# Performance work log

Hardware: AMD Instinct MI355X
Metric: run time of the kernel (lower is better)

Reference implementation:

```python
import jax, jax.numpy as jnp
import numpy as np

B, T, C = 2, 2048, 1024
H = 4 * C           # MLP hidden (4*n_embd)
E_DYN = 7           # num_experts - static_experts
TOP_K = 2           # num_experts_per_tok
MOE_LOSS_COEF = 0.01


def setup_inputs() -> dict:
    key = jax.random.key(0)
    ks = jax.random.split(key, 6)
    s = 0.02
    x = jax.random.normal(ks[0], (B, T, C), dtype=jnp.float32)
    gate_w = jax.random.normal(ks[1], (C, E_DYN), dtype=jnp.float32) * s
    w1 = jax.random.normal(ks[2], (E_DYN, C, H), dtype=jnp.float32) * s   # dynamic experts c_fc
    w2 = jax.random.normal(ks[3], (E_DYN, H, C), dtype=jnp.float32) * s   # dynamic experts c_proj
    w1s = jax.random.normal(ks[4], (C, H), dtype=jnp.float32) * s         # static expert c_fc
    w2s = jax.random.normal(ks[5], (H, C), dtype=jnp.float32) * s         # static expert c_proj
    return {"x": x, "gate_w": gate_w, "w1": w1, "w2": w2, "w1s": w1s, "w2s": w2s}


def reference(x, gate_w, w1, w2, w1s, w2s):
    b, t, c = x.shape
    xf = x.reshape(-1, c)                                   # [N, C]
    n = xf.shape[0]

    # static expert (always applied)
    y_static = jax.nn.gelu(xf @ w1s, approximate=False) @ w2s  # [N, C]

    # gating: top-k + softmax over selected scores
    scores = xf @ gate_w                                    # [N, E]
    topk_scores, topk_idx = jax.lax.top_k(scores, TOP_K)    # [N, K]
    topk_w = jax.nn.softmax(topk_scores, axis=-1)           # [N, K]

    # dense dispatch weights [N, E] (top_k indices are distinct -> set is safe)
    probs = jnp.zeros((n, E_DYN), dtype=x.dtype)
    probs = probs.at[jnp.arange(n)[:, None], topk_idx].set(topk_w)

    # all-expert MLP then weighted combine (same math as masked per-expert dispatch)
    h = jax.nn.gelu(jnp.einsum('nc,ech->enh', xf, w1), approximate=False)  # [E, N, H]
    y_all = jnp.einsum('enh,ehc->enc', h, w2)               # [E, N, C]
    y_dyn = jnp.einsum('ne,enc->nc', probs, y_all)          # [N, C]

    y = (y_dyn + y_static).reshape(b, t, c)

    # variance_penalty auxiliary loss
    expert_usage = probs.mean(axis=0)                       # [E]
    variance = jnp.mean((expert_usage - expert_usage.mean()) ** 2)
    aux = MOE_LOSS_COEF * variance
    return y, aux
```

## Files before the change

### kernel.cpp

```cpp
#include <hip/hip_runtime.h>
#include <hip/hip_bf16.h>
#include <math.h>

#define N_TOK 4096
#define C_DIM 1024
#define H_DIM 4096
#define NEXP 7
#define NGRP 8
#define HCAP 13184

typedef __attribute__((ext_vector_type(8))) short short8;
typedef __attribute__((ext_vector_type(4))) float floatx4;

static const size_t OFF_COUNTS = 0;
static const size_t OFF_CURSOR = 64;
static const size_t OFF_BASE   = 128;
static const size_t OFF_PCOUNT = 192;
static const size_t OFF_CNT8   = 256;
static const size_t OFF_USAGE  = 320;
static const size_t OFF_TOPKI  = 4096;
static const size_t OFF_TOPKW  = OFF_TOPKI + 8192ull * 4;
static const size_t OFF_ETOK   = OFF_TOPKW + 8192ull * 4;
static const size_t OFF_EWT    = OFF_ETOK + (size_t)HCAP * 4;
static const size_t OFF_XB     = 262144;
static const size_t OFF_W1T    = OFF_XB + (size_t)N_TOK * C_DIM * 2;
static const size_t OFF_W2T    = OFF_W1T + (size_t)NGRP * H_DIM * C_DIM * 2;
static const size_t OFF_H      = OFF_W2T + (size_t)NGRP * C_DIM * H_DIM * 2;

static __device__ __forceinline__ unsigned short f2bf(float f) {
    __hip_bfloat16 b = __float2bfloat16(f);
    return *reinterpret_cast<unsigned short*>(&b);
}

static __device__ __forceinline__ void gll16(const void* g, void* l) {
    __builtin_amdgcn_global_load_lds((const __attribute__((address_space(1))) void*)g,
                                     (__attribute__((address_space(3))) void*)l, 16, 0, 0);
}

__global__ void init_small_kernel(int* counts, int* cursor, float* usage) {
    int i = threadIdx.x;
    if (i < 8) { counts[i] = 0; cursor[i] = 0; usage[i] = 0.f; }
}

__global__ void zero_out_kernel(float* y, int n) {
    int i = blockIdx.x * blockDim.x + threadIdx.x;
    int stride = gridDim.x * blockDim.x;
    for (; i < n; i += stride) y[i] = 0.f;
}

__global__ void convert_x_kernel(const float* __restrict__ x, unsigned short* __restrict__ xb) {
    int i = blockIdx.x * 256 + threadIdx.x;
    float4 v = ((const float4*)x)[i];
    ushort4 o;
    o.x = f2bf(v.x); o.y = f2bf(v.y); o.z = f2bf(v.z); o.w = f2bf(v.w);
    ((ushort4*)xb)[i] = o;
}

__global__ __launch_bounds__(256) void transpose_cvt_kernel(
    const float* __restrict__ dyn, const float* __restrict__ stat,
    __hip_bfloat16* __restrict__ dst, int R, int S)
{
    int e = blockIdx.z;
    const float* src = (e < NEXP) ? (dyn + (size_t)e * R * S) : stat;
    __hip_bfloat16* d = dst + (size_t)e * R * S;
    int s0 = blockIdx.x * 32, r0 = blockIdx.y * 64;
    int tx = threadIdx.x & 31, ty = threadIdx.x >> 5;
    __shared__ float t[64][33];
#pragma unroll
    for (int i = 0; i < 8; i++) {
        int r = ty + i * 8;
        t[r][tx] = src[(size_t)(r0 + r) * S + s0 + tx];
    }
    __syncthreads();
    int tx2 = threadIdx.x & 63, ty2 = threadIdx.x >> 6;
#pragma unroll
    for (int i = 0; i < 8; i++) {
        int s = ty2 + i * 4;
        d[(size_t)(s0 + s) * R + r0 + tx2] = __float2bfloat16(t[tx2][s]);
    }
}

__global__ __launch_bounds__(256) void gate_kernel(
    const float* __restrict__ x, const float* __restrict__ gw,
    int* __restrict__ topki, float* __restrict__ topkw,
    int* counts, float* usage)
{
    int wid = threadIdx.x >> 6, lane = threadIdx.x & 63;
    int t = blockIdx.x * 4 + wid;
    float s[NEXP];
#pragma unroll
    for (int e = 0; e < NEXP; e++) s[e] = 0.f;
    for (int c = lane; c < C_DIM; c += 64) {
        float xv = x[(size_t)t * C_DIM + c];
#pragma unroll
        for (int e = 0; e < NEXP; e++) s[e] += xv * gw[c * NEXP + e];
    }
#pragma unroll
    for (int e = 0; e < NEXP; e++)
        for (int off = 32; off > 0; off >>= 1) s[e] += __shfl_xor(s[e], off);
    if (lane == 0) {
        int e0 = 0;
        for (int e = 1; e < NEXP; e++) if (s[e] > s[e0]) e0 = e;
        int e1 = -1;
        for (int e = 0; e < NEXP; e++) {
            if (e == e0) continue;
            if (e1 < 0 || s[e] > s[e1]) e1 = e;
        }
        float w0 = 1.f / (1.f + expf(s[e1] - s[e0]));
        float w1 = 1.f - w0;
        topki[t * 2] = e0; topki[t * 2 + 1] = e1;
        topkw[t * 2] = w0; topkw[t * 2 + 1] = w1;
        atomicAdd(&counts[e0], 1); atomicAdd(&counts[e1], 1);
        atomicAdd(&usage[e0], w0); atomicAdd(&usage[e1], w1);
    }
}

__global__ __launch_bounds__(256) void prefix_kernel(
    const int* counts, const float* usage,
    int* base, int* pcount, int* cnt8,
    int* etok, float* ewt, float* y, int aux_index)
{
    __shared__ int sb[NGRP], sc[NGRP], sp[NGRP];
    if (threadIdx.x == 0) {
        int run = 0;
        for (int g = 0; g < NEXP; g++) {
            int c = counts[g];
            int p = (c + 127) & ~127;
            base[g] = run; pcount[g] = p; cnt8[g] = c;
            sb[g] = run; sc[g] = c; sp[g] = p;
            run += p;
        }
        base[NEXP] = run; pcount[NEXP] = N_TOK; cnt8[NEXP] = N_TOK;
        sb[NEXP] = run; sc[NEXP] = N_TOK; sp[NEXP] = N_TOK;
        float u[NEXP]; float mean = 0.f;
        for (int e = 0; e < NEXP; e++) { u[e] = usage[e] / (float)N_TOK; mean += u[e]; }
        mean /= (float)NEXP;
        float var = 0.f;
        for (int e = 0; e < NEXP; e++) { float d = u[e] - mean; var += d * d; }
        var /= (float)NEXP;
        y[aux_index] = 0.01f * var;
    }
    __syncthreads();
    for (int i = threadIdx.x; i < N_TOK; i += 256) {
        etok[sb[NEXP] + i] = i; ewt[sb[NEXP] + i] = 1.0f;
    }
    for (int g = 0; g < NEXP; g++) {
        for (int i = sc[g] + (int)threadIdx.x; i < sp[g]; i += 256) {
            etok[sb[g] + i] = 0; ewt[sb[g] + i] = 0.f;
        }
    }
}

__global__ void scatter_kernel(const int* __restrict__ topki, const float* __restrict__ topkw,
                               const int* __restrict__ base, int* cursor,
                               int* __restrict__ etok, float* __restrict__ ewt)
{
    int i = blockIdx.x * 256 + threadIdx.x;
    int t = i >> 1;
    int e = topki[i];
    float w = topkw[i];
    int pos = atomicAdd(&cursor[e], 1);
    int idx = base[e] + pos;
    etok[idx] = t; ewt[idx] = w;
}

__global__ __launch_bounds__(256) void gemm1_kernel(
    const __hip_bfloat16* __restrict__ xb,
    const __hip_bfloat16* __restrict__ w1t,
    __hip_bfloat16* __restrict__ h,
    const int* __restrict__ etok,
    const int* __restrict__ base,
    const int* __restrict__ pcount)
{
    int g = blockIdx.z, mt = blockIdx.y, ct = blockIdx.x;
    if (mt * 128 >= pcount[g]) return;
    int eb = base[g];

    __shared__ __align__(16) char AlsB[2 * 8192];
    __shared__ __align__(16) char BlsB[2 * 8192];

    int tid = threadIdx.x;
    int lane = tid & 63, wid = tid >> 6;
    int quad = lane >> 4, l16 = lane & 15;
    int wm = wid >> 1, wn = wid & 1;
    int rsub = lane >> 2, chunk = lane & 3;

    const char* gA[2]; const char* gB[2];
    char* lA[2]; char* lB[2];
#pragma unroll
    for (int j = 0; j < 2; j++) {
        int rowA = wid * 32 + j * 16 + rsub;
        int tok = etok[eb + mt * 128 + rowA];
        gA[j] = (const char*)(xb + (size_t)tok * C_DIM) + chunk * 16;
        lA[j] = AlsB + (wid * 32 + j * 16) * 64;
        int rowB = wid * 32 + j * 16 + rsub;
        gB[j] = (const char*)(w1t + ((size_t)g * H_DIM + ct * 128 + rowB) * C_DIM) + chunk * 16;
        lB[j] = BlsB + (wid * 32 + j * 16) * 64;
    }

    floatx4 acc[4][4] = {};
    for (int k0 = 0; k0 < C_DIM; k0 += 64) {
        size_t koff = (size_t)k0 * 2;
#pragma unroll
        for (int s = 0; s < 2; s++) {
            size_t so = koff + (size_t)s * 64;
            gll16(gA[0] + so, lA[0] + s * 8192);
            gll16(gA[1] + so, lA[1] + s * 8192);
            gll16(gB[0] + so, lB[0] + s * 8192);
            gll16(gB[1] + so, lB[1] + s * 8192);
        }
        __syncthreads();
#pragma unroll
        for (int s = 0; s < 2; s++) {
            short8 a[4], b[4];
#pragma unroll
            for (int i = 0; i < 4; i++) {
                a[i] = *(const short8*)(AlsB + s * 8192 + (((wm * 64 + i * 16 + l16) * 32 + quad * 8) * 2));
                b[i] = *(const short8*)(BlsB + s * 8192 + (((wn * 64 + i * 16 + l16) * 32 + quad * 8) * 2));
            }
#pragma unroll
            for (int i = 0; i < 4; i++)
#pragma unroll
                for (int j = 0; j < 4; j++)
                    acc[i][j] = __builtin_amdgcn_mfma_f32_16x16x32_bf16(a[i], b[j], acc[i][j], 0, 0, 0);
        }
        __syncthreads();
    }

#pragma unroll
    for (int i = 0; i < 4; i++) {
        int rbase = mt * 128 + wm * 64 + i * 16 + quad * 4;
#pragma unroll
        for (int reg = 0; reg < 4; reg++) {
            size_t hrow = (size_t)(eb + rbase + reg) * H_DIM;
#pragma unroll
            for (int j = 0; j < 4; j++) {
                int cc = ct * 128 + wn * 64 + j * 16 + l16;
                float v = acc[i][j][reg];
                float ge = 0.5f * v * (1.0f + erff(v * 0.70710678118654752f));
                h[hrow + cc] = __float2bfloat16(ge);
            }
        }
    }
}

__global__ __launch_bounds__(256) void gemm2_kernel(
    const __hip_bfloat16* __restrict__ h,
    const __hip_bfloat16* __restrict__ w2t,
    float* __restrict__ y,
    const int* __restrict__ etok,
    const float* __restrict__ ewt,
    const int* __restrict__ base,
    const int* __restrict__ pcount,
    const int* __restrict__ cnt8)
{
    int g = blockIdx.z, ct = blockIdx.x, mt = blockIdx.y;
    if (mt * 128 >= pcount[g]) return;
    int eb = base[g];
    int cnt = cnt8[g];

    __shared__ __align__(16) char AlsB[2 * 8192];
    __shared__ __align__(16) char BlsB[2 * 8192];

    int tid = threadIdx.x;
    int lane = tid & 63, wid = tid >> 6;
    int quad = lane >> 4, l16 = lane & 15;
    int wm = wid >> 1, wn = wid & 1;
    int rsub = lane >> 2, chunk = lane & 3;

    const char* gA[2]; const char* gB[2];
    char* lA[2]; char* lB[2];
#pragma unroll
    for (int j = 0; j < 2; j++) {
        int rowA = wid * 32 + j * 16 + rsub;
        gA[j] = (const char*)(h + (size_t)(eb + mt * 128 + rowA) * H_DIM) + chunk * 16;
        lA[j] = AlsB + (wid * 32 + j * 16) * 64;
        int rowB = wid * 32 + j * 16 + rsub;
        gB[j] = (const char*)(w2t + ((size_t)g * C_DIM + ct * 128 + rowB) * H_DIM) + chunk * 16;
        lB[j] = BlsB + (wid * 32 + j * 16) * 64;
    }

    floatx4 acc[4][4] = {};
    for (int k0 = 0; k0 < H_DIM; k0 += 64) {
        size_t koff = (size_t)k0 * 2;
#pragma unroll
        for (int s = 0; s < 2; s++) {
            size_t so = koff + (size_t)s * 64;
            gll16(gA[0] + so, lA[0] + s * 8192);
            gll16(gA[1] + so, lA[1] + s * 8192);
            gll16(gB[0] + so, lB[0] + s * 8192);
            gll16(gB[1] + so, lB[1] + s * 8192);
        }
        __syncthreads();
#pragma unroll
        for (int s = 0; s < 2; s++) {
            short8 a[4], b[4];
#pragma unroll
            for (int i = 0; i < 4; i++) {
                a[i] = *(const short8*)(AlsB + s * 8192 + (((wm * 64 + i * 16 + l16) * 32 + quad * 8) * 2));
                b[i] = *(const short8*)(BlsB + s * 8192 + (((wn * 64 + i * 16 + l16) * 32 + quad * 8) * 2));
            }
#pragma unroll
            for (int i = 0; i < 4; i++)
#pragma unroll
                for (int j = 0; j < 4; j++)
                    acc[i][j] = __builtin_amdgcn_mfma_f32_16x16x32_bf16(a[i], b[j], acc[i][j], 0, 0, 0);
        }
        __syncthreads();
    }

#pragma unroll
    for (int i = 0; i < 4; i++) {
        int rl0 = mt * 128 + wm * 64 + i * 16 + quad * 4;
#pragma unroll
        for (int reg = 0; reg < 4; reg++) {
            int rl = rl0 + reg;
            if (rl < cnt) {
                int entry = eb + rl;
                float w = ewt[entry];
                int tok = etok[entry];
                size_t yrow = (size_t)tok * C_DIM;
#pragma unroll
                for (int j = 0; j < 4; j++) {
                    int cc = ct * 128 + wn * 64 + j * 16 + l16;
                    atomicAdd(&y[yrow + cc], acc[i][j][reg] * w);
                }
            }
        }
    }
}

extern "C" void kernel_launch(void* const* d_in, const int* in_sizes, int n_in,
                              void* d_out, int out_size, void* d_ws, size_t ws_size,
                              hipStream_t stream) {
    const float* x      = (const float*)d_in[0];
    const float* gate_w = (const float*)d_in[1];
    const float* w1     = (const float*)d_in[2];
    const float* w2     = (const float*)d_in[3];
    const float* w1s    = (const float*)d_in[4];
    const float* w2s    = (const float*)d_in[5];
    float* y = (float*)d_out;
    char* ws = (char*)d_ws;

    int*   counts = (int*)(ws + OFF_COUNTS);
    int*   cursor = (int*)(ws + OFF_CURSOR);
    int*   base   = (int*)(ws + OFF_BASE);
    int*   pcount = (int*)(ws + OFF_PCOUNT);
    int*   cnt8   = (int*)(ws + OFF_CNT8);
    float* usage  = (float*)(ws + OFF_USAGE);
    int*   topki  = (int*)(ws + OFF_TOPKI);
    float* topkw  = (float*)(ws + OFF_TOPKW);
    int*   etok   = (int*)(ws + OFF_ETOK);
    float* ewt    = (float*)(ws + OFF_EWT);
    unsigned short* xb_u = (unsigned short*)(ws + OFF_XB);
    __hip_bfloat16* xb  = (__hip_bfloat16*)(ws + OFF_XB);
    __hip_bfloat16* w1t = (__hip_bfloat16*)(ws + OFF_W1T);
    __hip_bfloat16* w2t = (__hip_bfloat16*)(ws + OFF_W2T);
    __hip_bfloat16* hbuf = (__hip_bfloat16*)(ws + OFF_H);

    init_small_kernel<<<1, 64, 0, stream>>>(counts, cursor, usage);
    zero_out_kernel<<<2048, 256, 0, stream>>>(y, out_size);

    convert_x_kernel<<<(N_TOK * C_DIM / 4) / 256, 256, 0, stream>>>(x, xb_u);
    transpose_cvt_kernel<<<dim3(H_DIM / 32, C_DIM / 64, NGRP), 256, 0, stream>>>(w1, w1s, w1t, C_DIM, H_DIM);
    transpose_cvt_kernel<<<dim3(C_DIM / 32, H_DIM / 64, NGRP), 256, 0, stream>>>(w2, w2s, w2t, H_DIM, C_DIM);

    gate_kernel<<<N_TOK / 4, 256, 0, stream>>>(x, gate_w, topki, topkw, counts, usage);
    prefix_kernel<<<1, 256, 0, stream>>>(counts, usage, base, pcount, cnt8, etok, ewt, y, N_TOK * C_DIM);
    scatter_kernel<<<(N_TOK * 2) / 256, 256, 0, stream>>>(topki, topkw, base, cursor, etok, ewt);

    gemm1_kernel<<<dim3(H_DIM / 128, 64, NGRP), 256, 0, stream>>>(xb, w1t, hbuf, etok, base, pcount);
    gemm2_kernel<<<dim3(C_DIM / 128, 64, NGRP), 256, 0, stream>>>(hbuf, w2t, y, etok, ewt, base, pcount, cnt8);
}
```

Baseline: 838.1 us.

## Replace atomic scatter-add in gemm2 with per-row partial writes and combine kernel

```diff
diff --git a/kernel.cpp b/kernel.cpp
--- a/kernel.cpp
+++ b/kernel.cpp
@@ -22,6 +22,7 @@
 static const size_t OFF_TOPKW  = OFF_TOPKI + 8192ull * 4;
 static const size_t OFF_ETOK   = OFF_TOPKW + 8192ull * 4;
 static const size_t OFF_EWT    = OFF_ETOK + (size_t)HCAP * 4;
+static const size_t OFF_EIDX   = OFF_EWT + (size_t)HCAP * 4;
 static const size_t OFF_XB     = 262144;
 static const size_t OFF_W1T    = OFF_XB + (size_t)N_TOK * C_DIM * 2;
 static const size_t OFF_W2T    = OFF_W1T + (size_t)NGRP * H_DIM * C_DIM * 2;
@@ -31,6 +32,21 @@
     __hip_bfloat16 b = __float2bfloat16(f);
     return *reinterpret_cast<unsigned short*>(&b);
 }
+static __device__ __forceinline__ float bf2f(unsigned short u) {
+    unsigned int v = ((unsigned int)u) << 16;
+    return __builtin_bit_cast(float, v);
+}
+
+static __device__ __forceinline__ float gelu_f(float v) {
+    float z = v * 0.70710678118654752f;
+    float az = fabsf(z);
+    float t = 1.0f / (1.0f + 0.3275911f * az);
+    float poly = t * (0.254829592f + t * (-0.284496736f + t * (1.421413741f +
+                 t * (-1.453152027f + t * 1.061405429f))));
+    float erf_abs = 1.0f - poly * __expf(-az * az);
+    float erf_v = (z < 0.f) ? -erf_abs : erf_abs;
+    return 0.5f * v * (1.0f + erf_v);
+}
 
 static __device__ __forceinline__ void gll16(const void* g, void* l) {
     __builtin_amdgcn_global_load_lds((const __attribute__((address_space(1))) void*)g,
@@ -40,12 +56,6 @@
 __global__ void init_small_kernel(int* counts, int* cursor, float* usage) {
     int i = threadIdx.x;
     if (i < 8) { counts[i] = 0; cursor[i] = 0; usage[i] = 0.f; }
-}
-
-__global__ void zero_out_kernel(float* y, int n) {
-    int i = blockIdx.x * blockDim.x + threadIdx.x;
-    int stride = gridDim.x * blockDim.x;
-    for (; i < n; i += stride) y[i] = 0.f;
 }
 
 __global__ void convert_x_kernel(const float* __restrict__ x, unsigned short* __restrict__ xb) {
@@ -153,7 +163,8 @@
 
 __global__ void scatter_kernel(const int* __restrict__ topki, const float* __restrict__ topkw,
                                const int* __restrict__ base, int* cursor,
-                               int* __restrict__ etok, float* __restrict__ ewt)
+                               int* __restrict__ etok, float* __restrict__ ewt,
+                               int* __restrict__ eidx)
 {
     int i = blockIdx.x * 256 + threadIdx.x;
     int t = i >> 1;
@@ -162,6 +173,7 @@
     int pos = atomicAdd(&cursor[e], 1);
     int idx = base[e] + pos;
     etok[idx] = t; ewt[idx] = w;
+    eidx[i] = idx;
 }
 
 __global__ __launch_bounds__(256) void gemm1_kernel(
@@ -236,9 +248,7 @@
 #pragma unroll
             for (int j = 0; j < 4; j++) {
                 int cc = ct * 128 + wn * 64 + j * 16 + l16;
-                float v = acc[i][j][reg];
-                float ge = 0.5f * v * (1.0f + erff(v * 0.70710678118654752f));
-                h[hrow + cc] = __float2bfloat16(ge);
+                h[hrow + cc] = __float2bfloat16(gelu_f(acc[i][j][reg]));
             }
         }
     }
@@ -247,17 +257,13 @@
 __global__ __launch_bounds__(256) void gemm2_kernel(
     const __hip_bfloat16* __restrict__ h,
     const __hip_bfloat16* __restrict__ w2t,
-    float* __restrict__ y,
-    const int* __restrict__ etok,
-    const float* __restrict__ ewt,
+    unsigned short* __restrict__ yp,
     const int* __restrict__ base,
-    const int* __restrict__ pcount,
-    const int* __restrict__ cnt8)
+    const int* __restrict__ pcount)
 {
     int g = blockIdx.z, ct = blockIdx.x, mt = blockIdx.y;
     if (mt * 128 >= pcount[g]) return;
     int eb = base[g];
-    int cnt = cnt8[g];
 
     __shared__ __align__(16) char AlsB[2 * 8192];
     __shared__ __align__(16) char BlsB[2 * 8192];
@@ -314,20 +320,37 @@
         int rl0 = mt * 128 + wm * 64 + i * 16 + quad * 4;
 #pragma unroll
         for (int reg = 0; reg < 4; reg++) {
-            int rl = rl0 + reg;
-            if (rl < cnt) {
-                int entry = eb + rl;
-                float w = ewt[entry];
-                int tok = etok[entry];
-                size_t yrow = (size_t)tok * C_DIM;
-#pragma unroll
-                for (int j = 0; j < 4; j++) {
-                    int cc = ct * 128 + wn * 64 + j * 16 + l16;
-                    atomicAdd(&y[yrow + cc], acc[i][j][reg] * w);
-                }
+            size_t yrow = (size_t)(eb + rl0 + reg) * C_DIM;
+#pragma unroll
+            for (int j = 0; j < 4; j++) {
+                int cc = ct * 128 + wn * 64 + j * 16 + l16;
+                yp[yrow + cc] = f2bf(acc[i][j][reg]);
             }
         }
     }
+}
+
+__global__ __launch_bounds__(256) void combine_kernel(
+    const unsigned short* __restrict__ yp,
+    const int* __restrict__ eidx,
+    const float* __restrict__ topkw,
+    const int* __restrict__ base,
+    float* __restrict__ y)
+{
+    int t = blockIdx.x;
+    int i0 = eidx[t * 2], i1 = eidx[t * 2 + 1];
+    float w0 = topkw[t * 2], w1 = topkw[t * 2 + 1];
+    int is = base[NEXP] + t;
+    int c = threadIdx.x * 4;
+    ushort4 a = *(const ushort4*)(yp + (size_t)i0 * C_DIM + c);
+    ushort4 b = *(const ushort4*)(yp + (size_t)i1 * C_DIM + c);
+    ushort4 s = *(const ushort4*)(yp + (size_t)is * C_DIM + c);
+    float4 o;
+    o.x = w0 * bf2f(a.x) + w1 * bf2f(b.x) + bf2f(s.x);
+    o.y = w0 * bf2f(a.y) + w1 * bf2f(b.y) + bf2f(s.y);
+    o.z = w0 * bf2f(a.z) + w1 * bf2f(b.z) + bf2f(s.z);
+    o.w = w0 * bf2f(a.w) + w1 * bf2f(b.w) + bf2f(s.w);
+    *(float4*)(y + (size_t)t * C_DIM + c) = o;
 }
 
 extern "C" void kernel_launch(void* const* d_in, const int* in_sizes, int n_in,
@@ -352,14 +375,15 @@
     float* topkw  = (float*)(ws + OFF_TOPKW);
     int*   etok   = (int*)(ws + OFF_ETOK);
     float* ewt    = (float*)(ws + OFF_EWT);
+    int*   eidx   = (int*)(ws + OFF_EIDX);
     unsigned short* xb_u = (unsigned short*)(ws + OFF_XB);
     __hip_bfloat16* xb  = (__hip_bfloat16*)(ws + OFF_XB);
     __hip_bfloat16* w1t = (__hip_bfloat16*)(ws + OFF_W1T);
     __hip_bfloat16* w2t = (__hip_bfloat16*)(ws + OFF_W2T);
     __hip_bfloat16* hbuf = (__hip_bfloat16*)(ws + OFF_H);
+    unsigned short* yp  = (unsigned short*)(ws + OFF_W1T);
 
     init_small_kernel<<<1, 64, 0, stream>>>(counts, cursor, usage);
-    zero_out_kernel<<<2048, 256, 0, stream>>>(y, out_size);
 
     convert_x_kernel<<<(N_TOK * C_DIM / 4) / 256, 256, 0, stream>>>(x, xb_u);
     transpose_cvt_kernel<<<dim3(H_DIM / 32, C_DIM / 64, NGRP), 256, 0, stream>>>(w1, w1s, w1t, C_DIM, H_DIM);
@@ -367,8 +391,9 @@
 
     gate_kernel<<<N_TOK / 4, 256, 0, stream>>>(x, gate_w, topki, topkw, counts, usage);
     prefix_kernel<<<1, 256, 0, stream>>>(counts, usage, base, pcount, cnt8, etok, ewt, y, N_TOK * C_DIM);
-    scatter_kernel<<<(N_TOK * 2) / 256, 256, 0, stream>>>(topki, topkw, base, cursor, etok, ewt);
+    scatter_kernel<<<(N_TOK * 2) / 256, 256, 0, stream>>>(topki, topkw, base, cursor, etok, ewt, eidx);
 
     gemm1_kernel<<<dim3(H_DIM / 128, 64, NGRP), 256, 0, stream>>>(xb, w1t, hbuf, etok, base, pcount);
-    gemm2_kernel<<<dim3(C_DIM / 128, 64, NGRP), 256, 0, stream>>>(hbuf, w2t, y, etok, ewt, base, pcount, cnt8);
-}
+    gemm2_kernel<<<dim3(C_DIM / 128, 64, NGRP), 256, 0, stream>>>(hbuf, w2t, yp, base, pcount);
+    combine_kernel<<<N_TOK, 256, 0, stream>>>(yp, eidx, topkw, base, y);
+}
```

New measurement: 818.6 us. 1.02x faster.
